# Kernel tuning notes

Measured on AMD Instinct MI355X. Metric: run time of the kernel, lower is better.

## Reference

```python
import jax, jax.numpy as jnp
import numpy as np

LN_EPS = 1e-5
L2_EPS = 1e-12
SCALE = 8.0

def setup_inputs() -> dict:
    key = jax.random.key(0)
    k0, k1, k2 = jax.random.split(key, 3)
    b, c, H, W = 16, 256, 64, 64
    heads, dim_head = 8, 32
    dim_inner = heads * dim_head  # 256
    x = jax.random.normal(k0, (b, c, H, W), dtype=jnp.float32)
    ln_gamma = jnp.ones((c,), jnp.float32)
    ln_beta = jnp.zeros((c,), jnp.float32)
    W_qkv = jax.random.normal(k1, (c, 3 * dim_inner), dtype=jnp.float32) * 0.02
    temperature = jnp.ones((heads,), jnp.float32)
    W_out = jax.random.normal(k2, (dim_inner, c), dtype=jnp.float32) * 0.02
    b_out = jnp.zeros((c,), jnp.float32)
    return {"x": x, "ln_gamma": ln_gamma, "ln_beta": ln_beta, "W_qkv": W_qkv,
            "temperature": temperature, "W_out": W_out, "b_out": b_out, "heads": heads}

def _l2norm(t):
    # F.normalize(t, dim=-1): divide by clamped L2 norm along last axis
    n = jnp.sqrt(jnp.sum(t * t, axis=-1, keepdims=True))
    return t / jnp.maximum(n, L2_EPS)

def reference(x, ln_gamma, ln_beta, W_qkv, temperature, W_out, b_out, heads):
    b, c, H, W = x.shape
    n = H * W
    dim_head = W_qkv.shape[1] // (3 * heads)
    # b c h w -> b (h w) c
    t = jnp.transpose(x, (0, 2, 3, 1)).reshape(b, n, c)
    # LayerNorm over channel dim (affine)
    mu = jnp.mean(t, axis=-1, keepdims=True)
    var = jnp.mean(jnp.square(t - mu), axis=-1, keepdims=True)
    t = (t - mu) * jax.lax.rsqrt(var + LN_EPS) * ln_gamma + ln_beta
    # qkv projection; split last dim as (qkv, heads, dim_head) -> (3, b, h, d, n)
    qkv = (t @ W_qkv).reshape(b, n, 3, heads, dim_head)
    qkv = jnp.transpose(qkv, (2, 0, 3, 4, 1))
    q, k, v = qkv[0], qkv[1], qkv[2]
    q = _l2norm(q) * jnp.exp(temperature)[None, :, None, None]
    k = _l2norm(k)
    # cross-covariance attention over channel dim: sim is [b, h, d, d]
    sim = jnp.einsum('bhin,bhjn->bhij', q, k) * SCALE
    attn = jax.nn.softmax(sim, axis=-1)
    out = jnp.einsum('bhij,bhjn->bhin', attn, v)  # [b, h, d, n]
    # b h d n -> b n (h d)
    out = jnp.transpose(out, (0, 3, 1, 2)).reshape(b, n, heads * dim_head)
    out = out @ W_out + b_out
    # b (h w) c -> b c h w
    return jnp.transpose(out.reshape(b, H, W, c), (0, 3, 1, 2))
```

## Files before the change

### kernel.cpp

```cpp
#include <hip/hip_runtime.h>

typedef unsigned short u16;
typedef __bf16 bf16x8 __attribute__((ext_vector_type(8)));
typedef float f32x4 __attribute__((ext_vector_type(4)));

#define MFMA(a, b, c) __builtin_amdgcn_mfma_f32_16x16x32_bf16((a), (b), (c), 0, 0, 0)

__device__ __forceinline__ u16 f2bf(float f) {
    unsigned u = __float_as_uint(f);
    unsigned r = (u + 0x7fffu + ((u >> 16) & 1u)) >> 16;
    return (u16)r;
}
__device__ __forceinline__ float bf2f(u16 h) { return __uint_as_float(((unsigned)h) << 16); }


__global__ __launch_bounds__(256) void k_ln(const float* __restrict__ x,
                                            const float* __restrict__ gamma,
                                            const float* __restrict__ beta,
                                            u16* __restrict__ xlnT) {
    int bid = blockIdx.x;
    int b = bid >> 6, nt = bid & 63;
    int nb = nt * 64;
    __shared__ unsigned xsu[256 * 33];
    __shared__ float muv[64], rsv[64];
    __shared__ float redS[8 * 64], redS2[8 * 64];
    int t = threadIdx.x;
    {
        int np = t & 31;
        int c0 = t >> 5;
        const float* xp = x + ((size_t)b * 256) * 4096 + nb + np * 2;
        for (int i = 0; i < 32; i++) {
            int c = c0 + i * 8;
            float2 f = *(const float2*)(xp + (size_t)c * 4096);
            unsigned u = (unsigned)f2bf(f.x) | ((unsigned)f2bf(f.y) << 16);
            xsu[c * 33 + np] = u;
        }
    }
    __syncthreads();
    {
        int np = t & 31, q = t >> 5;
        float s0 = 0, s20 = 0, s1 = 0, s21 = 0;
        for (int i = 0; i < 32; i++) {
            unsigned u = xsu[(q * 32 + i) * 33 + np];
            float a = bf2f((u16)(u & 0xffffu));
            float bv = bf2f((u16)(u >> 16));
            s0 += a; s20 += a * a; s1 += bv; s21 += bv * bv;
        }
        redS[q * 64 + np * 2] = s0;  redS[q * 64 + np * 2 + 1] = s1;
        redS2[q * 64 + np * 2] = s20; redS2[q * 64 + np * 2 + 1] = s21;
    }
    __syncthreads();
    if (t < 64) {
        float s = 0, s2 = 0;
        for (int q = 0; q < 8; q++) { s += redS[q * 64 + t]; s2 += redS2[q * 64 + t]; }
        float m = s * (1.f / 256.f);
        float var = s2 * (1.f / 256.f) - m * m;
        muv[t] = m;
        rsv[t] = rsqrtf(var + 1e-5f);
    }
    __syncthreads();
    {
        int c4 = (t & 63) * 4;
        int ng = t >> 6;
        float g[4], e[4];
        for (int j = 0; j < 4; j++) { g[j] = gamma[c4 + j]; e[j] = beta[c4 + j]; }
        for (int i = 0; i < 16; i++) {
            int n = ng * 16 + i;
            float m = muv[n], rs = rsv[n];
            u16 h[4];
            for (int j = 0; j < 4; j++) {
                unsigned u = xsu[(c4 + j) * 33 + (n >> 1)];
                u16 raw = (n & 1) ? (u16)(u >> 16) : (u16)(u & 0xffffu);
                float v = (bf2f(raw) - m) * rs * g[j] + e[j];
                h[j] = f2bf(v);
            }
            uint2 w2;
            w2.x = (unsigned)h[0] | ((unsigned)h[1] << 16);
            w2.y = (unsigned)h[2] | ((unsigned)h[3] << 16);
            *(uint2*)(xlnT + ((size_t)(b * 4096 + nb + n)) * 256 + c4) = w2;
        }
    }
}

__global__ __launch_bounds__(256) void k_prep(const float* __restrict__ Wqkv,
                                              const float* __restrict__ Wout,
                                              u16* __restrict__ WqkvT, u16* __restrict__ WoutT,
                                              float* __restrict__ sims) {
    int i = blockIdx.x * 256 + threadIdx.x;
    if (i < 768 * 256) { int o = i >> 8, c = i & 255; WqkvT[i] = f2bf(Wqkv[c * 768 + o]); }
    if (i < 256 * 256) { int o = i >> 8, c = i & 255; WoutT[i] = f2bf(Wout[c * 256 + o]); }
    if (i < 128 * 1024) sims[i] = 0.f;
}

__global__ __launch_bounds__(256) void k_gemm(const u16* __restrict__ A, const u16* __restrict__ Bb,
                                              int mtiles, u16* __restrict__ o16,
                                              float* __restrict__ o32, const float* __restrict__ bias,
                                              int mode) {
    int bid = blockIdx.x;
    int per_b = mtiles * 32;
    int b = bid / per_b;
    int r2 = bid % per_b;
    int mbase = (r2 >> 5) * 128, nbase = (r2 & 31) * 128;
    __shared__ u16 aT[128 * 40];
    __shared__ u16 bT[128 * 40];
    int t = threadIdx.x, w = t >> 6, lane = t & 63, l15 = lane & 15, quad = lane >> 4;
    const u16* Bp = Bb + (size_t)b * 4096 * 256;
    f32x4 acc[2][8];
    f32x4 z = {0.f, 0.f, 0.f, 0.f};
    for (int fm = 0; fm < 2; fm++)
        for (int fn = 0; fn < 8; fn++) acc[fm][fn] = z;
    int arow = t >> 1, ac = (t & 1) * 16;
    for (int kt = 0; kt < 8; kt++) {
        int kb = kt * 32;
        if (kt) __syncthreads();
        {
            const uint4* g = (const uint4*)(A + (size_t)(mbase + arow) * 256 + kb + ac);
            uint4 p0 = g[0], p1 = g[1];
            *(uint4*)&aT[arow * 40 + ac] = p0;
            *(uint4*)&aT[arow * 40 + ac + 8] = p1;
        }
        {
            const uint4* g = (const uint4*)(Bp + (size_t)(nbase + arow) * 256 + kb + ac);
            uint4 p0 = g[0], p1 = g[1];
            *(uint4*)&bT[arow * 40 + ac] = p0;
            *(uint4*)&bT[arow * 40 + ac + 8] = p1;
        }
        __syncthreads();
        bf16x8 af0 = *(const bf16x8*)&aT[(w * 32 + l15) * 40 + quad * 8];
        bf16x8 af1 = *(const bf16x8*)&aT[(w * 32 + 16 + l15) * 40 + quad * 8];
        for (int fn = 0; fn < 8; fn++) {
            bf16x8 bfr = *(const bf16x8*)&bT[(fn * 16 + l15) * 40 + quad * 8];
            acc[0][fn] = MFMA(af0, bfr, acc[0][fn]);
            acc[1][fn] = MFMA(af1, bfr, acc[1][fn]);
        }
    }
    for (int fm = 0; fm < 2; fm++)
        for (int fn = 0; fn < 8; fn++)
            for (int r = 0; r < 4; r++) {
                int row = mbase + w * 32 + fm * 16 + quad * 4 + r;
                int col = nbase + fn * 16 + l15;
                float v = acc[fm][fn][r];
                if (mode == 0)
                    o16[((size_t)b * 768 + row) * 4096 + col] = f2bf(v);
                else
                    o32[((size_t)b * 256 + row) * 4096 + col] = v + bias[row];
            }
}

__global__ __launch_bounds__(256) void k_norms(const u16* __restrict__ qkv, float* __restrict__ normsq) {
    int bid = blockIdx.x;
    int b = bid >> 6, rg = bid & 63;
    int t = threadIdx.x;
    int r8 = t >> 5, l32 = t & 31;
    int o = rg * 8 + r8;
    const u16* p = qkv + ((size_t)b * 768 + o) * 4096 + l32 * 8;
    float s = 0.f;
    for (int i = 0; i < 16; i++) {
        uint4 u = *(const uint4*)(p + i * 256);
        const u16* us = (const u16*)&u;
        for (int jj = 0; jj < 8; jj++) { float f = bf2f(us[jj]); s += f * f; }
    }
    s += __shfl_down(s, 16, 32);
    s += __shfl_down(s, 8, 32);
    s += __shfl_down(s, 4, 32);
    s += __shfl_down(s, 2, 32);
    s += __shfl_down(s, 1, 32);
    if (l32 == 0) normsq[b * 512 + o] = s;
}

__global__ __launch_bounds__(256) void k_sim(const u16* __restrict__ qkv, float* __restrict__ sims) {
    int bid = blockIdx.x;
    int bh = bid >> 1, half = bid & 1;
    int b = bh >> 3, h = bh & 7;
    __shared__ u16 qs[32 * 264];
    __shared__ u16 ks[32 * 264];
    int t = threadIdx.x, w = t >> 6, lane = t & 63, l15 = lane & 15, quad = lane >> 4;
    int ib = w >> 1, jb = w & 1;
    const u16* qbase = qkv + ((size_t)(b * 768) + h * 32) * 4096;
    const u16* kbase = qkv + ((size_t)(b * 768) + 256 + h * 32) * 4096;
    int col8 = t & 31, rb = t >> 5;
    f32x4 acc = {0.f, 0.f, 0.f, 0.f};
    for (int kc = 0; kc < 8; kc++) {
        int kb = half * 2048 + kc * 256;
        __syncthreads();
        for (int i = 0; i < 4; i++) {
            int r = rb + i * 8;
            uint4 pq = *(const uint4*)(qbase + (size_t)r * 4096 + kb + col8 * 8);
            *(uint4*)&qs[r * 264 + col8 * 8] = pq;
            uint4 pk = *(const uint4*)(kbase + (size_t)r * 4096 + kb + col8 * 8);
            *(uint4*)&ks[r * 264 + col8 * 8] = pk;
        }
        __syncthreads();
        for (int s = 0; s < 8; s++) {
            bf16x8 a = *(const bf16x8*)&qs[(ib * 16 + l15) * 264 + s * 32 + quad * 8];
            bf16x8 bb = *(const bf16x8*)&ks[(jb * 16 + l15) * 264 + s * 32 + quad * 8];
            acc = MFMA(a, bb, acc);
        }
    }
    float* sp = sims + (size_t)bh * 1024;
    for (int r = 0; r < 4; r++) {
        int row = ib * 16 + quad * 4 + r, col = jb * 16 + l15;
        atomicAdd(sp + row * 32 + col, acc[r]);
    }
}

__global__ __launch_bounds__(64) void k_soft(const float* __restrict__ sims,
                                             const float* __restrict__ normsq,
                                             const float* __restrict__ temp, u16* __restrict__ attn) {
    int bh = blockIdx.x;
    int b = bh >> 3, h = bh & 7;
    __shared__ float scq[32], sck[32];
    int t = threadIdx.x;
    if (t < 32)
        scq[t] = expf(temp[h]) * 8.0f / fmaxf(sqrtf(normsq[b * 512 + h * 32 + t]), 1e-12f);
    else {
        int d = t - 32;
        sck[d] = 1.0f / fmaxf(sqrtf(normsq[b * 512 + 256 + h * 32 + d]), 1e-12f);
    }
    __syncthreads();
    if (t < 32) {
        float row[32];
        float m = -1e30f;
        const float* sp = sims + (size_t)bh * 1024 + t * 32;
        float sq = scq[t];
        for (int j = 0; j < 32; j++) { float v = sp[j] * sq * sck[j]; row[j] = v; m = fmaxf(m, v); }
        float s = 0.f;
        for (int j = 0; j < 32; j++) { float p = expf(row[j] - m); row[j] = p; s += p; }
        float inv = 1.f / s;
        u16* ap = attn + (size_t)bh * 1024 + t * 32;
        for (int j = 0; j < 32; j++) ap[j] = f2bf(row[j] * inv);
    }
}

__global__ __launch_bounds__(256) void k_pv(const u16* __restrict__ qkv, const u16* __restrict__ attn,
                                            u16* __restrict__ oaT) {
    int bid = blockIdx.x;
    int nc = bid & 15, h = (bid >> 4) & 7, b = bid >> 7;
    int nb = nc * 256;
    __shared__ u16 vt[256 * 40];
    int t = threadIdx.x, w = t >> 6, lane = t & 63, l15 = lane & 15, quad = lane >> 4;
    const u16* ap = attn + (size_t)(b * 8 + h) * 1024;
    bf16x8 a0 = *(const bf16x8*)(ap + l15 * 32 + quad * 8);
    bf16x8 a1 = *(const bf16x8*)(ap + (16 + l15) * 32 + quad * 8);
    const u16* vp = qkv + ((size_t)(b * 768) + 512 + h * 32) * 4096 + nb;
    int col8 = t & 31, rb = t >> 5;
    for (int i = 0; i < 4; i++) {
        int j = rb + i * 8;
        uint4 p = *(const uint4*)(vp + (size_t)j * 4096 + col8 * 8);
        const u16* us = (const u16*)&p;
        int ch = j >> 3;
        for (int jj = 0; jj < 8; jj++) {
            int nl = col8 * 8 + jj;
            vt[nl * 40 + ((ch ^ (col8 & 3)) << 3) + (j & 7)] = us[jj];
        }
    }
    __syncthreads();
    f32x4 z = {0.f, 0.f, 0.f, 0.f};
    for (int mm = 0; mm < 4; mm++) {
        int nlb = (w * 4 + mm) * 16;
        int nl = nlb + l15;
        bf16x8 vf = *(const bf16x8*)&vt[nl * 40 + ((quad ^ ((nl >> 3) & 3)) << 3)];
        f32x4 d0 = MFMA(vf, a0, z);
        f32x4 d1 = MFMA(vf, a1, z);
        for (int r = 0; r < 4; r++) {
            int n = nb + nlb + quad * 4 + r;
            size_t base = ((size_t)(b * 4096) + n) * 256 + h * 32;
            oaT[base + l15] = f2bf(d0[r]);
            oaT[base + 16 + l15] = f2bf(d1[r]);
        }
    }
}

extern "C" void kernel_launch(void* const* d_in, const int* in_sizes, int n_in,
                              void* d_out, int out_size, void* d_ws, size_t ws_size,
                              hipStream_t stream) {
    const float* x     = (const float*)d_in[0];
    const float* gamma = (const float*)d_in[1];
    const float* beta  = (const float*)d_in[2];
    const float* Wqkv  = (const float*)d_in[3];
    const float* temp  = (const float*)d_in[4];
    const float* Wout  = (const float*)d_in[5];
    const float* bout  = (const float*)d_in[6];
    float* out = (float*)d_out;

    char* ws = (char*)d_ws;
    size_t off = 0;
    auto alloc = [&](size_t nbytes) -> void* {
        void* p = ws + off;
        off = (off + nbytes + 255) & ~(size_t)255;
        return p;
    };
    u16* xlnT    = (u16*)alloc((size_t)16 * 4096 * 256 * 2);
    u16* WqkvT   = (u16*)alloc((size_t)768 * 256 * 2);
    u16* WoutT   = (u16*)alloc((size_t)256 * 256 * 2);
    u16* qkv     = (u16*)alloc((size_t)16 * 768 * 4096 * 2);
    float* normsq = (float*)alloc((size_t)16 * 512 * 4);
    float* sims   = (float*)alloc((size_t)128 * 1024 * 4);
    u16* attn    = (u16*)alloc((size_t)128 * 1024 * 2);
    u16* oaT     = (u16*)alloc((size_t)16 * 4096 * 256 * 2);
    (void)ws_size; (void)in_sizes; (void)n_in; (void)out_size;

    hipLaunchKernelGGL(k_ln, dim3(1024), dim3(256), 0, stream, x, gamma, beta, xlnT);
    hipLaunchKernelGGL(k_prep, dim3(768), dim3(256), 0, stream, Wqkv, Wout, WqkvT, WoutT, sims);
    hipLaunchKernelGGL(k_gemm, dim3(3072), dim3(256), 0, stream, WqkvT, xlnT, 6,
                       qkv, (float*)nullptr, (const float*)nullptr, 0);
    hipLaunchKernelGGL(k_norms, dim3(1024), dim3(256), 0, stream, qkv, normsq);
    hipLaunchKernelGGL(k_sim, dim3(256), dim3(256), 0, stream, qkv, sims);
    hipLaunchKernelGGL(k_soft, dim3(128), dim3(64), 0, stream, sims, normsq, temp, attn);
    hipLaunchKernelGGL(k_pv, dim3(2048), dim3(256), 0, stream, qkv, attn, oaT);
    hipLaunchKernelGGL(k_gemm, dim3(1024), dim3(256), 0, stream, WoutT, oaT, 2,
                       (u16*)nullptr, out, bout, 1);
}
```

Measured before the change: 261.4 us.

## Fold attention into output projection, fuse norms into QKV GEMM epilogue

The attn·V step and the output projection are reassociated into a per-batch matrix M2 = W_out·attn, built by a small kernel, so one GEMM over a transposed V replaces the separate PV kernel and the oaT intermediate. The QKV GEMM now keeps the weight fragments in registers, stages wider K tiles in LDS, computes the q/k squared norms in its epilogue with atomics, and writes coalesced q/k rows plus a transposed V through shared memory. k_sim reads global memory directly with finer K splits. This removes the norms pass and a full activation round trip, at the cost of more atomics and extra bf16 rounding in M2.

```diff
diff --git a/kernel.cpp b/kernel.cpp
--- a/kernel.cpp
+++ b/kernel.cpp
@@ -85,128 +85,147 @@
 __global__ __launch_bounds__(256) void k_prep(const float* __restrict__ Wqkv,
                                               const float* __restrict__ Wout,
                                               u16* __restrict__ WqkvT, u16* __restrict__ WoutT,
-                                              float* __restrict__ sims) {
+                                              float* __restrict__ sims, float* __restrict__ normsq) {
     int i = blockIdx.x * 256 + threadIdx.x;
     if (i < 768 * 256) { int o = i >> 8, c = i & 255; WqkvT[i] = f2bf(Wqkv[c * 768 + o]); }
     if (i < 256 * 256) { int o = i >> 8, c = i & 255; WoutT[i] = f2bf(Wout[c * 256 + o]); }
     if (i < 128 * 1024) sims[i] = 0.f;
-}
-
-__global__ __launch_bounds__(256) void k_gemm(const u16* __restrict__ A, const u16* __restrict__ Bb,
-                                              int mtiles, u16* __restrict__ o16,
-                                              float* __restrict__ o32, const float* __restrict__ bias,
-                                              int mode) {
+    if (i < 16 * 512) normsq[i] = 0.f;
+}
+
+__global__ __launch_bounds__(256, 3) void k_qkv(const u16* __restrict__ WqkvT,
+                                                const u16* __restrict__ xlnT,
+                                                u16* __restrict__ qkv, u16* __restrict__ vT,
+                                                float* __restrict__ normsq) {
     int bid = blockIdx.x;
-    int per_b = mtiles * 32;
-    int b = bid / per_b;
-    int r2 = bid % per_b;
-    int mbase = (r2 >> 5) * 128, nbase = (r2 & 31) * 128;
-    __shared__ u16 aT[128 * 40];
-    __shared__ u16 bT[128 * 40];
+    int b = bid / 192, r0 = bid % 192;
+    int mt = r0 >> 5, nt = r0 & 31;
+    int mbase = mt * 128, nbase = nt * 128;
+    __shared__ __align__(16) u16 smem[128 * 136];
     int t = threadIdx.x, w = t >> 6, lane = t & 63, l15 = lane & 15, quad = lane >> 4;
-    const u16* Bp = Bb + (size_t)b * 4096 * 256;
+    bf16x8 afr[2][8];
+#pragma unroll
+    for (int fm = 0; fm < 2; fm++)
+#pragma unroll
+        for (int kt = 0; kt < 8; kt++)
+            afr[fm][kt] = *(const bf16x8*)(WqkvT + (size_t)(mbase + w * 32 + fm * 16 + l15) * 256 + kt * 32 + quad * 8);
     f32x4 acc[2][8];
     f32x4 z = {0.f, 0.f, 0.f, 0.f};
+#pragma unroll
     for (int fm = 0; fm < 2; fm++)
+#pragma unroll
         for (int fn = 0; fn < 8; fn++) acc[fm][fn] = z;
-    int arow = t >> 1, ac = (t & 1) * 16;
-    for (int kt = 0; kt < 8; kt++) {
-        int kb = kt * 32;
-        if (kt) __syncthreads();
+    const u16* Bp = xlnT + ((size_t)b * 4096 + nbase) * 256;
+    int srow = t >> 1, sseg = t & 1;
+    for (int h = 0; h < 2; h++) {
+        if (h) __syncthreads();
+#pragma unroll
+        for (int g = 0; g < 2; g++) {
+            uint4 ld[4];
+#pragma unroll
+            for (int i = 0; i < 4; i++)
+                ld[i] = *(const uint4*)(Bp + (size_t)srow * 256 + h * 128 + sseg * 64 + g * 32 + i * 8);
+#pragma unroll
+            for (int i = 0; i < 4; i++)
+                *(uint4*)&smem[srow * 136 + sseg * 64 + g * 32 + i * 8] = ld[i];
+        }
+        __syncthreads();
+#pragma unroll
+        for (int ktl = 0; ktl < 4; ktl++) {
+            int kt = h * 4 + ktl;
+#pragma unroll
+            for (int fn = 0; fn < 8; fn++) {
+                bf16x8 bfr = *(const bf16x8*)&smem[(fn * 16 + l15) * 136 + ktl * 32 + quad * 8];
+                acc[0][fn] = MFMA(afr[0][kt], bfr, acc[0][fn]);
+                acc[1][fn] = MFMA(afr[1][kt], bfr, acc[1][fn]);
+            }
+        }
+    }
+    __syncthreads();
+    if (mt < 4) {
+#pragma unroll
+        for (int fm = 0; fm < 2; fm++)
+#pragma unroll
+            for (int rr = 0; rr < 4; rr++) {
+                float s = 0.f;
+#pragma unroll
+                for (int fn = 0; fn < 8; fn++) { float v = acc[fm][fn][rr]; s += v * v; }
+                s += __shfl_down(s, 8, 16);
+                s += __shfl_down(s, 4, 16);
+                s += __shfl_down(s, 2, 16);
+                s += __shfl_down(s, 1, 16);
+                if (l15 == 0)
+                    atomicAdd(&normsq[b * 512 + mbase + w * 32 + fm * 16 + quad * 4 + rr], s);
+            }
+#pragma unroll
+        for (int fm = 0; fm < 2; fm++)
+#pragma unroll
+            for (int fn = 0; fn < 8; fn++)
+#pragma unroll
+                for (int rr = 0; rr < 4; rr++) {
+                    int ml = w * 32 + fm * 16 + quad * 4 + rr;
+                    smem[ml * 136 + fn * 16 + l15] = f2bf(acc[fm][fn][rr]);
+                }
+        __syncthreads();
         {
-            const uint4* g = (const uint4*)(A + (size_t)(mbase + arow) * 256 + kb + ac);
-            uint4 p0 = g[0], p1 = g[1];
-            *(uint4*)&aT[arow * 40 + ac] = p0;
-            *(uint4*)&aT[arow * 40 + ac + 8] = p1;
-        }
+            int ml = t >> 1, seg = t & 1;
+            u16* dst = qkv + ((size_t)b * 512 + mbase + ml) * 4096 + nbase + seg * 64;
+#pragma unroll
+            for (int i = 0; i < 8; i++) {
+                uint4 u = *(const uint4*)&smem[ml * 136 + seg * 64 + i * 8];
+                *(uint4*)(dst + i * 8) = u;
+            }
+        }
+    } else {
+#pragma unroll
+        for (int fm = 0; fm < 2; fm++)
+#pragma unroll
+            for (int fn = 0; fn < 8; fn++)
+#pragma unroll
+                for (int rr = 0; rr < 4; rr++) {
+                    int ml = w * 32 + fm * 16 + quad * 4 + rr;
+                    int col = fn * 16 + l15;
+                    smem[col * 136 + ml] = f2bf(acc[fm][fn][rr]);
+                }
+        __syncthreads();
         {
-            const uint4* g = (const uint4*)(Bp + (size_t)(nbase + arow) * 256 + kb + ac);
-            uint4 p0 = g[0], p1 = g[1];
-            *(uint4*)&bT[arow * 40 + ac] = p0;
-            *(uint4*)&bT[arow * 40 + ac + 8] = p1;
-        }
-        __syncthreads();
-        bf16x8 af0 = *(const bf16x8*)&aT[(w * 32 + l15) * 40 + quad * 8];
-        bf16x8 af1 = *(const bf16x8*)&aT[(w * 32 + 16 + l15) * 40 + quad * 8];
-        for (int fn = 0; fn < 8; fn++) {
-            bf16x8 bfr = *(const bf16x8*)&bT[(fn * 16 + l15) * 40 + quad * 8];
-            acc[0][fn] = MFMA(af0, bfr, acc[0][fn]);
-            acc[1][fn] = MFMA(af1, bfr, acc[1][fn]);
-        }
-    }
-    for (int fm = 0; fm < 2; fm++)
-        for (int fn = 0; fn < 8; fn++)
-            for (int r = 0; r < 4; r++) {
-                int row = mbase + w * 32 + fm * 16 + quad * 4 + r;
-                int col = nbase + fn * 16 + l15;
-                float v = acc[fm][fn][r];
-                if (mode == 0)
-                    o16[((size_t)b * 768 + row) * 4096 + col] = f2bf(v);
-                else
-                    o32[((size_t)b * 256 + row) * 4096 + col] = v + bias[row];
-            }
-}
-
-__global__ __launch_bounds__(256) void k_norms(const u16* __restrict__ qkv, float* __restrict__ normsq) {
-    int bid = blockIdx.x;
-    int b = bid >> 6, rg = bid & 63;
-    int t = threadIdx.x;
-    int r8 = t >> 5, l32 = t & 31;
-    int o = rg * 8 + r8;
-    const u16* p = qkv + ((size_t)b * 768 + o) * 4096 + l32 * 8;
-    float s = 0.f;
-    for (int i = 0; i < 16; i++) {
-        uint4 u = *(const uint4*)(p + i * 256);
-        const u16* us = (const u16*)&u;
-        for (int jj = 0; jj < 8; jj++) { float f = bf2f(us[jj]); s += f * f; }
-    }
-    s += __shfl_down(s, 16, 32);
-    s += __shfl_down(s, 8, 32);
-    s += __shfl_down(s, 4, 32);
-    s += __shfl_down(s, 2, 32);
-    s += __shfl_down(s, 1, 32);
-    if (l32 == 0) normsq[b * 512 + o] = s;
+            int nl = t >> 1, seg = t & 1;
+            int dbase = mbase - 512;
+            u16* dst = vT + ((size_t)b * 4096 + nbase + nl) * 256 + dbase + seg * 64;
+#pragma unroll
+            for (int i = 0; i < 8; i++) {
+                uint4 u = *(const uint4*)&smem[nl * 136 + seg * 64 + i * 8];
+                *(uint4*)(dst + i * 8) = u;
+            }
+        }
+    }
 }
 
 __global__ __launch_bounds__(256) void k_sim(const u16* __restrict__ qkv, float* __restrict__ sims) {
     int bid = blockIdx.x;
-    int bh = bid >> 1, half = bid & 1;
+    int kc = bid & 15, bh = bid >> 4;
     int b = bh >> 3, h = bh & 7;
-    __shared__ u16 qs[32 * 264];
-    __shared__ u16 ks[32 * 264];
     int t = threadIdx.x, w = t >> 6, lane = t & 63, l15 = lane & 15, quad = lane >> 4;
     int ib = w >> 1, jb = w & 1;
-    const u16* qbase = qkv + ((size_t)(b * 768) + h * 32) * 4096;
-    const u16* kbase = qkv + ((size_t)(b * 768) + 256 + h * 32) * 4096;
-    int col8 = t & 31, rb = t >> 5;
+    const u16* qb = qkv + ((size_t)b * 512 + h * 32 + ib * 16 + l15) * 4096 + kc * 256 + quad * 8;
+    const u16* kb = qkv + ((size_t)b * 512 + 256 + h * 32 + jb * 16 + l15) * 4096 + kc * 256 + quad * 8;
     f32x4 acc = {0.f, 0.f, 0.f, 0.f};
-    for (int kc = 0; kc < 8; kc++) {
-        int kb = half * 2048 + kc * 256;
-        __syncthreads();
-        for (int i = 0; i < 4; i++) {
-            int r = rb + i * 8;
-            uint4 pq = *(const uint4*)(qbase + (size_t)r * 4096 + kb + col8 * 8);
-            *(uint4*)&qs[r * 264 + col8 * 8] = pq;
-            uint4 pk = *(const uint4*)(kbase + (size_t)r * 4096 + kb + col8 * 8);
-            *(uint4*)&ks[r * 264 + col8 * 8] = pk;
-        }
-        __syncthreads();
-        for (int s = 0; s < 8; s++) {
-            bf16x8 a = *(const bf16x8*)&qs[(ib * 16 + l15) * 264 + s * 32 + quad * 8];
-            bf16x8 bb = *(const bf16x8*)&ks[(jb * 16 + l15) * 264 + s * 32 + quad * 8];
-            acc = MFMA(a, bb, acc);
-        }
+#pragma unroll
+    for (int s = 0; s < 8; s++) {
+        bf16x8 qf = *(const bf16x8*)(qb + s * 32);
+        bf16x8 kf = *(const bf16x8*)(kb + s * 32);
+        acc = MFMA(qf, kf, acc);
     }
     float* sp = sims + (size_t)bh * 1024;
-    for (int r = 0; r < 4; r++) {
-        int row = ib * 16 + quad * 4 + r, col = jb * 16 + l15;
-        atomicAdd(sp + row * 32 + col, acc[r]);
-    }
+#pragma unroll
+    for (int rr = 0; rr < 4; rr++)
+        atomicAdd(sp + (ib * 16 + quad * 4 + rr) * 32 + jb * 16 + l15, acc[rr]);
 }
 
 __global__ __launch_bounds__(64) void k_soft(const float* __restrict__ sims,
                                              const float* __restrict__ normsq,
-                                             const float* __restrict__ temp, u16* __restrict__ attn) {
+                                             const float* __restrict__ temp,
+                                             u16* __restrict__ attn, u16* __restrict__ attnT) {
     int bh = blockIdx.x;
     int b = bh >> 3, h = bh & 7;
     __shared__ float scq[32], sck[32];
@@ -228,45 +247,111 @@
         for (int j = 0; j < 32; j++) { float p = expf(row[j] - m); row[j] = p; s += p; }
         float inv = 1.f / s;
         u16* ap = attn + (size_t)bh * 1024 + t * 32;
-        for (int j = 0; j < 32; j++) ap[j] = f2bf(row[j] * inv);
-    }
-}
-
-__global__ __launch_bounds__(256) void k_pv(const u16* __restrict__ qkv, const u16* __restrict__ attn,
-                                            u16* __restrict__ oaT) {
+        u16* apT = attnT + (size_t)bh * 1024;
+        for (int j = 0; j < 32; j++) {
+            u16 hv = f2bf(row[j] * inv);
+            ap[j] = hv;
+            apT[j * 32 + t] = hv;
+        }
+    }
+}
+
+__global__ __launch_bounds__(256) void k_m2(const u16* __restrict__ WoutT,
+                                            const u16* __restrict__ attnT, u16* __restrict__ M2) {
+    int bh = blockIdx.x;
+    int b = bh >> 3, h = bh & 7;
+    int t = threadIdx.x, w = t >> 6, lane = t & 63, l15 = lane & 15, quad = lane >> 4;
+    const u16* at = attnT + (size_t)bh * 1024;
+    bf16x8 bf0 = *(const bf16x8*)(at + l15 * 32 + quad * 8);
+    bf16x8 bf1 = *(const bf16x8*)(at + (16 + l15) * 32 + quad * 8);
+    f32x4 z = {0.f, 0.f, 0.f, 0.f};
+#pragma unroll
+    for (int fm = 0; fm < 4; fm++) {
+        bf16x8 af = *(const bf16x8*)(WoutT + (size_t)(w * 64 + fm * 16 + l15) * 256 + h * 32 + quad * 8);
+        f32x4 d0 = MFMA(af, bf0, z);
+        f32x4 d1 = MFMA(af, bf1, z);
+#pragma unroll
+        for (int rr = 0; rr < 4; rr++) {
+            int c = w * 64 + fm * 16 + quad * 4 + rr;
+            u16* mp = M2 + ((size_t)b * 256 + c) * 256 + h * 32;
+            mp[l15] = f2bf(d0[rr]);
+            mp[16 + l15] = f2bf(d1[rr]);
+        }
+    }
+}
+
+__global__ __launch_bounds__(256, 3) void k_out(const u16* __restrict__ M2,
+                                                const u16* __restrict__ vT,
+                                                const float* __restrict__ bias,
+                                                float* __restrict__ out) {
     int bid = blockIdx.x;
-    int nc = bid & 15, h = (bid >> 4) & 7, b = bid >> 7;
-    int nb = nc * 256;
-    __shared__ u16 vt[256 * 40];
+    int b = bid >> 6, r0 = bid & 63;
+    int mt = r0 >> 5, nt = r0 & 31;
+    int mbase = mt * 128, nbase = nt * 128;
+    __shared__ __align__(16) u16 smem[128 * 136];
+    float* smf = (float*)smem;
     int t = threadIdx.x, w = t >> 6, lane = t & 63, l15 = lane & 15, quad = lane >> 4;
-    const u16* ap = attn + (size_t)(b * 8 + h) * 1024;
-    bf16x8 a0 = *(const bf16x8*)(ap + l15 * 32 + quad * 8);
-    bf16x8 a1 = *(const bf16x8*)(ap + (16 + l15) * 32 + quad * 8);
-    const u16* vp = qkv + ((size_t)(b * 768) + 512 + h * 32) * 4096 + nb;
-    int col8 = t & 31, rb = t >> 5;
-    for (int i = 0; i < 4; i++) {
-        int j = rb + i * 8;
-        uint4 p = *(const uint4*)(vp + (size_t)j * 4096 + col8 * 8);
-        const u16* us = (const u16*)&p;
-        int ch = j >> 3;
-        for (int jj = 0; jj < 8; jj++) {
-            int nl = col8 * 8 + jj;
-            vt[nl * 40 + ((ch ^ (col8 & 3)) << 3) + (j & 7)] = us[jj];
-        }
-    }
-    __syncthreads();
+    bf16x8 afr[2][8];
+#pragma unroll
+    for (int fm = 0; fm < 2; fm++)
+#pragma unroll
+        for (int kt = 0; kt < 8; kt++)
+            afr[fm][kt] = *(const bf16x8*)(M2 + ((size_t)b * 256 + mbase + w * 32 + fm * 16 + l15) * 256 + kt * 32 + quad * 8);
+    f32x4 acc[2][8];
     f32x4 z = {0.f, 0.f, 0.f, 0.f};
-    for (int mm = 0; mm < 4; mm++) {
-        int nlb = (w * 4 + mm) * 16;
-        int nl = nlb + l15;
-        bf16x8 vf = *(const bf16x8*)&vt[nl * 40 + ((quad ^ ((nl >> 3) & 3)) << 3)];
-        f32x4 d0 = MFMA(vf, a0, z);
-        f32x4 d1 = MFMA(vf, a1, z);
-        for (int r = 0; r < 4; r++) {
-            int n = nb + nlb + quad * 4 + r;
-            size_t base = ((size_t)(b * 4096) + n) * 256 + h * 32;
-            oaT[base + l15] = f2bf(d0[r]);
-            oaT[base + 16 + l15] = f2bf(d1[r]);
+#pragma unroll
+    for (int fm = 0; fm < 2; fm++)
+#pragma unroll
+        for (int fn = 0; fn < 8; fn++) acc[fm][fn] = z;
+    const u16* Bp = vT + ((size_t)b * 4096 + nbase) * 256;
+    int srow = t >> 1, sseg = t & 1;
+    for (int h = 0; h < 2; h++) {
+        if (h) __syncthreads();
+#pragma unroll
+        for (int g = 0; g < 2; g++) {
+            uint4 ld[4];
+#pragma unroll
+            for (int i = 0; i < 4; i++)
+                ld[i] = *(const uint4*)(Bp + (size_t)srow * 256 + h * 128 + sseg * 64 + g * 32 + i * 8);
+#pragma unroll
+            for (int i = 0; i < 4; i++)
+                *(uint4*)&smem[srow * 136 + sseg * 64 + g * 32 + i * 8] = ld[i];
+        }
+        __syncthreads();
+#pragma unroll
+        for (int ktl = 0; ktl < 4; ktl++) {
+            int kt = h * 4 + ktl;
+#pragma unroll
+            for (int fn = 0; fn < 8; fn++) {
+                bf16x8 bfr = *(const bf16x8*)&smem[(fn * 16 + l15) * 136 + ktl * 32 + quad * 8];
+                acc[0][fn] = MFMA(afr[0][kt], bfr, acc[0][fn]);
+                acc[1][fn] = MFMA(afr[1][kt], bfr, acc[1][fn]);
+            }
+        }
+    }
+#pragma unroll
+    for (int nh = 0; nh < 2; nh++) {
+        __syncthreads();
+#pragma unroll
+        for (int fm = 0; fm < 2; fm++)
+#pragma unroll
+            for (int fnh = 0; fnh < 4; fnh++)
+#pragma unroll
+                for (int rr = 0; rr < 4; rr++) {
+                    int ml = w * 32 + fm * 16 + quad * 4 + rr;
+                    smf[ml * 68 + fnh * 16 + l15] = acc[fm][nh * 4 + fnh][rr];
+                }
+        __syncthreads();
+        {
+            int ml = t >> 1, seg = t & 1;
+            float bs = bias[mbase + ml];
+            float* dst = out + ((size_t)b * 256 + mbase + ml) * 4096 + nbase + nh * 64 + seg * 32;
+#pragma unroll
+            for (int i = 0; i < 8; i++) {
+                float4 v = *(const float4*)&smf[ml * 68 + seg * 32 + i * 4];
+                v.x += bs; v.y += bs; v.z += bs; v.w += bs;
+                *(float4*)(dst + i * 4) = v;
+            }
         }
     }
 }
@@ -290,24 +375,23 @@
         off = (off + nbytes + 255) & ~(size_t)255;
         return p;
     };
-    u16* xlnT    = (u16*)alloc((size_t)16 * 4096 * 256 * 2);
-    u16* WqkvT   = (u16*)alloc((size_t)768 * 256 * 2);
-    u16* WoutT   = (u16*)alloc((size_t)256 * 256 * 2);
-    u16* qkv     = (u16*)alloc((size_t)16 * 768 * 4096 * 2);
+    u16* xlnT     = (u16*)alloc((size_t)16 * 4096 * 256 * 2);
+    u16* WqkvT    = (u16*)alloc((size_t)768 * 256 * 2);
+    u16* WoutT    = (u16*)alloc((size_t)256 * 256 * 2);
+    u16* qkv      = (u16*)alloc((size_t)16 * 512 * 4096 * 2);
+    u16* vT       = (u16*)alloc((size_t)16 * 4096 * 256 * 2);
     float* normsq = (float*)alloc((size_t)16 * 512 * 4);
     float* sims   = (float*)alloc((size_t)128 * 1024 * 4);
-    u16* attn    = (u16*)alloc((size_t)128 * 1024 * 2);
-    u16* oaT     = (u16*)alloc((size_t)16 * 4096 * 256 * 2);
+    u16* attn     = (u16*)alloc((size_t)128 * 1024 * 2);
+    u16* attnT    = (u16*)alloc((size_t)128 * 1024 * 2);
+    u16* M2       = (u16*)alloc((size_t)16 * 256 * 256 * 2);
     (void)ws_size; (void)in_sizes; (void)n_in; (void)out_size;
 
     hipLaunchKernelGGL(k_ln, dim3(1024), dim3(256), 0, stream, x, gamma, beta, xlnT);
-    hipLaunchKernelGGL(k_prep, dim3(768), dim3(256), 0, stream, Wqkv, Wout, WqkvT, WoutT, sims);
-    hipLaunchKernelGGL(k_gemm, dim3(3072), dim3(256), 0, stream, WqkvT, xlnT, 6,
-                       qkv, (float*)nullptr, (const float*)nullptr, 0);
-    hipLaunchKernelGGL(k_norms, dim3(1024), dim3(256), 0, stream, qkv, normsq);
-    hipLaunchKernelGGL(k_sim, dim3(256), dim3(256), 0, stream, qkv, sims);
-    hipLaunchKernelGGL(k_soft, dim3(128), dim3(64), 0, stream, sims, normsq, temp, attn);
-    hipLaunchKernelGGL(k_pv, dim3(2048), dim3(256), 0, stream, qkv, attn, oaT);
-    hipLaunchKernelGGL(k_gemm, dim3(1024), dim3(256), 0, stream, WoutT, oaT, 2,
-                       (u16*)nullptr, out, bout, 1);
-}
+    hipLaunchKernelGGL(k_prep, dim3(768), dim3(256), 0, stream, Wqkv, Wout, WqkvT, WoutT, sims, normsq);
+    hipLaunchKernelGGL(k_qkv, dim3(3072), dim3(256), 0, stream, WqkvT, xlnT, qkv, vT, normsq);
+    hipLaunchKernelGGL(k_sim, dim3(2048), dim3(256), 0, stream, qkv, sims);
+    hipLaunchKernelGGL(k_soft, dim3(128), dim3(64), 0, stream, sims, normsq, temp, attn, attnT);
+    hipLaunchKernelGGL(k_m2, dim3(128), dim3(256), 0, stream, WoutT, attnT, M2);
+    hipLaunchKernelGGL(k_out, dim3(1024), dim3(256), 0, stream, M2, vT, bout, out);
+}
```

Measured after the change: 305.1 us. +16.7%, slower.
